# Performance work log

Hardware: AMD Instinct MI355X
Metric: run time of the kernel (lower is better)

## Reference

```python
import jax, jax.numpy as jnp
import numpy as np

EMB = 1024
B, N = 4, 2048


def setup_inputs() -> dict:
    key = jax.random.key(0)
    ks = jax.random.split(key, 10)
    s = 1.0 / np.sqrt(EMB)
    return {
        "x": jax.random.normal(ks[0], (B, N, EMB), dtype=jnp.float32),
        "Wq": jax.random.normal(ks[1], (EMB, EMB), dtype=jnp.float32) * s,
        "bq": jnp.zeros((EMB,), dtype=jnp.float32),
        "Wk": jax.random.normal(ks[2], (EMB, EMB), dtype=jnp.float32) * s,
        "bk": jnp.zeros((EMB,), dtype=jnp.float32),
        "Wv": jax.random.normal(ks[3], (EMB, EMB), dtype=jnp.float32) * s,
        "bv": jnp.zeros((EMB,), dtype=jnp.float32),
        "Wm": jax.random.normal(ks[4], (EMB, EMB), dtype=jnp.float32) * s,
        "bm": jnp.zeros((EMB,), dtype=jnp.float32),
    }


def reference(x, Wq, bq, Wk, bk, Wv, bv, Wm, bm):
    # Projections (torch Linear: x @ W^T + b; here W is stored pre-transposed)
    q = x @ Wq + bq  # [B,N,D]
    k = x @ Wk + bk
    v = x @ Wv + bv
    # scores[b,i,j] = q[b,i,:] . k[b,j,:]  (no 1/sqrt(d) scaling in original)
    scores = jnp.einsum("bid,bjd->bij", q, k)
    # NOTE: softmax over dim=1 (the query/i axis), as in the original
    alpha = jax.nn.softmax(scores, axis=1)  # [B,N,N]
    # t[b,j,d] = sum_i v[b,i,d] * alpha[b,i,j]  == alpha^T @ v per batch
    t = jnp.einsum("bij,bid->bjd", alpha, v)  # [B,N,D]
    # MLP(emb, emb, []) is a single Linear, followed by outer relu
    return jax.nn.relu(t @ Wm + bm)
```

## Files before the change

kernel.cpp:

```cpp
#include <hip/hip_runtime.h>
#include <hip/hip_bf16.h>
#include <hip/hip_fp16.h>
#include <math.h>

#define EMB 1024
#define SEQ 2048
#define BATCH 4

typedef _Float16 half8 __attribute__((ext_vector_type(8)));
typedef float floatx4 __attribute__((ext_vector_type(4)));

__device__ __forceinline__ void gload_lds16(const void* g, void* l) {
    __builtin_amdgcn_global_load_lds(
        (const __attribute__((address_space(1))) void*)g,
        (__attribute__((address_space(3))) void*)l, 16, 0, 0);
}

__device__ __forceinline__ void sbar() {
    __builtin_amdgcn_sched_barrier(0);
    __builtin_amdgcn_s_barrier();
    __builtin_amdgcn_sched_barrier(0);
}

template <int EPI>
__global__ __launch_bounds__(512) void gemm_8p(
    const _Float16* __restrict__ A, const _Float16* __restrict__ B,
    void* __restrict__ Cv, const float* __restrict__ bias,
    int M, int N, int K, long sAb, long sBb, long sCb) {
    __shared__ _Float16 lds[3 * 24576];
    const int tid = threadIdx.x;
    const int lane = tid & 63;
    const int wave = tid >> 6;
    const long zb = blockIdx.z;
    A += zb * sAb;
    B += zb * sBb;
    const int bm = blockIdx.x * 256;
    const int bn = blockIdx.y * 128;
    floatx4 acc[4][4];
#pragma unroll
    for (int mi = 0; mi < 4; ++mi)
#pragma unroll
        for (int ni = 0; ni < 4; ++ni) acc[mi][ni] = (floatx4){0.f, 0.f, 0.f, 0.f};

    const int srow = tid >> 3;
    const int ssl = (tid & 7) ^ (srow & 7);
    const _Float16* Ag = A + (long)(bm + srow) * K + ssl * 8;
    const _Float16* Bg = B + (long)(bn + srow) * K + ssl * 8;
    const long K64 = (long)K * 64;
    const int ldst = wave * 512;

    const int wm = (wave >> 1) * 64;
    const int wn = (wave & 1) * 64;
    const int l15 = lane & 15;
    const int x7 = lane & 7;
    const int g4 = lane >> 4;
    const int sl0 = (g4 ^ x7) * 8;
    const int sl1 = ((4 + g4) ^ x7) * 8;
    const int fA0 = (wm + l15) * 64 + sl0;
    const int fA1 = (wm + l15) * 64 + sl1;
    const int fB0 = 16384 + (wn + l15) * 64 + sl0;
    const int fB1 = 16384 + (wn + l15) * 64 + sl1;

#define STG_H0(kt_, so_)                                                       \
    gload_lds16(Ag + (kt_), &lds[(so_) + ldst]);                               \
    gload_lds16(Ag + K64 + (kt_), &lds[(so_) + 4096 + ldst]);                  \
    gload_lds16(Bg + (kt_), &lds[(so_) + 16384 + ldst]);
#define STG_H1(kt_, so_)                                                       \
    gload_lds16(Ag + 2 * K64 + (kt_), &lds[(so_) + 8192 + ldst]);              \
    gload_lds16(Ag + 3 * K64 + (kt_), &lds[(so_) + 12288 + ldst]);             \
    gload_lds16(Bg + K64 + (kt_), &lds[(so_) + 16384 + 4096 + ldst]);

#define PHASE(fa_, fb_, co_, STG_)                                             \
    {                                                                          \
        half8 af[4], bf[4];                                                    \
        _Pragma("unroll") for (int mi = 0; mi < 4; ++mi)                       \
            af[mi] = *(const half8*)&lds[(co_) + (fa_) + mi * 1024];           \
        _Pragma("unroll") for (int ni = 0; ni < 4; ++ni)                       \
            bf[ni] = *(const half8*)&lds[(co_) + (fb_) + ni * 1024];           \
        STG_                                                                   \
        sbar();                                                                \
        asm volatile("s_waitcnt lgkmcnt(0)" ::: "memory");                     \
        __builtin_amdgcn_sched_barrier(0);                                     \
        __builtin_amdgcn_s_setprio(1);                                         \
        _Pragma("unroll") for (int mi = 0; mi < 4; ++mi)                       \
            _Pragma("unroll") for (int ni = 0; ni < 4; ++ni)                   \
                acc[mi][ni] = __builtin_amdgcn_mfma_f32_16x16x32_f16(          \
                    af[mi], bf[ni], acc[mi][ni], 0, 0, 0);                     \
        __builtin_amdgcn_s_setprio(0);                                         \
    }

#define TILE_END(n_)                                                           \
    __builtin_amdgcn_sched_barrier(0);                                         \
    asm volatile("s_waitcnt vmcnt(" #n_ ")" ::: "memory");                     \
    __builtin_amdgcn_s_barrier();                                              \
    __builtin_amdgcn_sched_barrier(0);

    STG_H0(0, 0) STG_H1(0, 0)
    STG_H0(64, 24576) STG_H1(64, 24576)
    TILE_END(6)
    int co = 0, so = 49152;
    const int NT = K >> 6;
    for (int t = 0; t < NT - 2; ++t) {
        const long kt2 = (long)(t + 2) << 6;
        PHASE(fA0, fB0, co, STG_H0(kt2, so))
        sbar();
        PHASE(fA1, fB1, co, STG_H1(kt2, so))
        TILE_END(6)
        co += 24576; if (co == 73728) co = 0;
        so += 24576; if (so == 73728) so = 0;
    }
    PHASE(fA0, fB0, co, )
    sbar();
    PHASE(fA1, fB1, co, )
    TILE_END(0)
    co += 24576; if (co == 73728) co = 0;
    PHASE(fA0, fB0, co, )
    sbar();
    PHASE(fA1, fB1, co, )
#undef STG_H0
#undef STG_H1
#undef PHASE
#undef TILE_END

    const int er = (lane >> 4) * 4;
    const int ec = lane & 15;
#pragma unroll
    for (int mi = 0; mi < 4; ++mi) {
#pragma unroll
        for (int ni = 0; ni < 4; ++ni) {
            const int col = bn + wn + ni * 16 + ec;
#pragma unroll
            for (int r = 0; r < 4; ++r) {
                const int row = bm + wm + mi * 16 + er + r;
                float v = acc[mi][ni][r];
                if (EPI == 0 || EPI == 1 || EPI == 3) v += bias[col];
                if (EPI == 3) v = fmaxf(v, 0.f);
                if (EPI == 0 || EPI == 4) {
                    ((_Float16*)Cv)[zb * sCb + (long)row * N + col] = (_Float16)v;
                } else if (EPI == 1) {
                    const long b = row >> 11;
                    const long i = row & (SEQ - 1);
                    ((_Float16*)Cv)[(b * EMB + col) * SEQ + i] = (_Float16)v;
                } else {
                    ((float*)Cv)[zb * sCb + (long)row * N + col] = v;
                }
            }
        }
    }
}

__global__ __launch_bounds__(256) void softmax_rows(const float* __restrict__ P,
                                                    _Float16* __restrict__ Aout) {
    const long row = blockIdx.x;
    const float* p = P + row * (long)SEQ;
    const int tid = threadIdx.x;
    float4 x0 = ((const float4*)p)[2 * tid];
    float4 x1 = ((const float4*)p)[2 * tid + 1];
    float v[8] = {x0.x, x0.y, x0.z, x0.w, x1.x, x1.y, x1.z, x1.w};
    float m = v[0];
#pragma unroll
    for (int j = 1; j < 8; ++j) m = fmaxf(m, v[j]);
#pragma unroll
    for (int o = 32; o; o >>= 1) m = fmaxf(m, __shfl_xor(m, o));
    __shared__ float rbuf[4];
    __shared__ float sbuf[4];
    const int lane = tid & 63, wv = tid >> 6;
    if (!lane) rbuf[wv] = m;
    __syncthreads();
    m = fmaxf(fmaxf(rbuf[0], rbuf[1]), fmaxf(rbuf[2], rbuf[3]));
    float s = 0.f;
#pragma unroll
    for (int j = 0; j < 8; ++j) {
        v[j] = expf(v[j] - m);
        s += v[j];
    }
#pragma unroll
    for (int o = 32; o; o >>= 1) s += __shfl_xor(s, o);
    if (!lane) sbuf[wv] = s;
    __syncthreads();
    s = sbuf[0] + sbuf[1] + sbuf[2] + sbuf[3];
    const float inv = 1.f / s;
    half8 h;
#pragma unroll
    for (int j = 0; j < 8; ++j) h[j] = (_Float16)(v[j] * inv);
    *(half8*)(Aout + row * (long)SEQ + tid * 8) = h;
}

__global__ __launch_bounds__(256) void cast_x(const float* __restrict__ X,
                                              _Float16* __restrict__ Xh) {
    const long i = (long)(blockIdx.x * 256 + threadIdx.x) * 8;
    float4 a = ((const float4*)(X + i))[0];
    float4 b = ((const float4*)(X + i))[1];
    half8 h;
    h[0] = (_Float16)a.x; h[1] = (_Float16)a.y; h[2] = (_Float16)a.z; h[3] = (_Float16)a.w;
    h[4] = (_Float16)b.x; h[5] = (_Float16)b.y; h[6] = (_Float16)b.z; h[7] = (_Float16)b.w;
    *(half8*)(Xh + i) = h;
}

__global__ __launch_bounds__(256) void transpose_cast(const float* __restrict__ W,
                                                      _Float16* __restrict__ Wt) {
    __shared__ float tile[32][33];
    const int bx = blockIdx.x * 32;
    const int by = blockIdx.y * 32;
    const int tx = threadIdx.x, ty = threadIdx.y;
#pragma unroll
    for (int r = 0; r < 32; r += 8)
        tile[ty + r][tx] = W[(long)(by + ty + r) * EMB + bx + tx];
    __syncthreads();
#pragma unroll
    for (int r = 0; r < 32; r += 8)
        Wt[(long)(bx + ty + r) * EMB + by + tx] = (_Float16)tile[tx][ty + r];
}

extern "C" void kernel_launch(void* const* d_in, const int* in_sizes, int n_in,
                              void* d_out, int out_size, void* d_ws, size_t ws_size,
                              hipStream_t stream) {
    const float* x  = (const float*)d_in[0];
    const float* Wq = (const float*)d_in[1];
    const float* bq = (const float*)d_in[2];
    const float* Wk = (const float*)d_in[3];
    const float* bk = (const float*)d_in[4];
    const float* Wv = (const float*)d_in[5];
    const float* bv = (const float*)d_in[6];
    const float* Wm = (const float*)d_in[7];
    const float* bm = (const float*)d_in[8];
    float* out = (float*)d_out;

    char* ws = (char*)d_ws;
    const long MB = 1l << 20;
    _Float16* xh  = (_Float16*)(ws + 0 * MB);
    _Float16* wqt = (_Float16*)(ws + 16 * MB);
    _Float16* wkt = (_Float16*)(ws + 18 * MB);
    _Float16* wvt = (_Float16*)(ws + 20 * MB);
    _Float16* wmt = (_Float16*)(ws + 22 * MB);
    _Float16* q   = (_Float16*)(ws + 24 * MB);
    _Float16* k   = (_Float16*)(ws + 40 * MB);
    _Float16* vt  = (_Float16*)(ws + 56 * MB);
    _Float16* t   = (_Float16*)(ws + 72 * MB);
    float*    P   = (float*)(ws + 88 * MB);
    _Float16* al  = (_Float16*)(ws + 152 * MB);

    const long MN = (long)BATCH * SEQ;

    cast_x<<<4096, 256, 0, stream>>>(x, xh);
    transpose_cast<<<dim3(32, 32), dim3(32, 8), 0, stream>>>(Wq, wqt);
    transpose_cast<<<dim3(32, 32), dim3(32, 8), 0, stream>>>(Wk, wkt);
    transpose_cast<<<dim3(32, 32), dim3(32, 8), 0, stream>>>(Wv, wvt);
    transpose_cast<<<dim3(32, 32), dim3(32, 8), 0, stream>>>(Wm, wmt);

    gemm_8p<0><<<dim3(32, 8), 512, 0, stream>>>(xh, wqt, q, bq, (int)MN, EMB, EMB, 0, 0, 0);
    gemm_8p<0><<<dim3(32, 8), 512, 0, stream>>>(xh, wkt, k, bk, (int)MN, EMB, EMB, 0, 0, 0);
    gemm_8p<1><<<dim3(32, 8), 512, 0, stream>>>(xh, wvt, vt, bv, (int)MN, EMB, EMB, 0, 0, 0);

    gemm_8p<2><<<dim3(8, 16, BATCH), 512, 0, stream>>>(
        k, q, P, nullptr, SEQ, SEQ, EMB,
        (long)SEQ * EMB, (long)SEQ * EMB, (long)SEQ * SEQ);

    softmax_rows<<<BATCH * SEQ, 256, 0, stream>>>(P, al);

    gemm_8p<4><<<dim3(8, 8, BATCH), 512, 0, stream>>>(
        al, vt, t, nullptr, SEQ, EMB, SEQ,
        (long)SEQ * SEQ, (long)EMB * SEQ, (long)SEQ * EMB);

    gemm_8p<3><<<dim3(32, 8), 512, 0, stream>>>(t, wmt, out, bm, (int)MN, EMB, EMB, 0, 0, 0);
}
```

Measured before the change: 303.3 us.

## Use 256x256 tile GEMM kernel for attention score and value GEMMs

Adds a new gemm256 kernel with a 256x256 output tile per 512-thread block, a 4-stage LDS ring filled by direct global-to-LDS loads with swizzled columns, and K-tile 32. The two batched attention GEMMs (scores and alpha^T·V) switch to it, so each block gets more data reuse and fewer blocks need to be launched. In exchange each thread holds a larger accumulator and the grid is smaller (256 and 128 blocks), which may leave some CUs idle and raise register pressure.

```diff
diff --git a/kernel.cpp b/kernel.cpp
--- a/kernel.cpp
+++ b/kernel.cpp
@@ -20,6 +20,117 @@
     __builtin_amdgcn_sched_barrier(0);
     __builtin_amdgcn_s_barrier();
     __builtin_amdgcn_sched_barrier(0);
+}
+
+template <int EPI>
+__global__ __launch_bounds__(512, 2) void gemm256(
+    const _Float16* __restrict__ A, const _Float16* __restrict__ B,
+    void* __restrict__ Cv, const float* __restrict__ bias,
+    int M, int N, int K, long sAb, long sBb, long sCb) {
+    __shared__ _Float16 lds[65536];
+    const int tid = threadIdx.x;
+    const int lane = tid & 63;
+    const int wave = tid >> 6;
+    const long zb = blockIdx.z;
+    A += zb * sAb;
+    B += zb * sBb;
+    const int bm = blockIdx.x * 256;
+    const int bn = blockIdx.y * 256;
+    floatx4 acc[8][4];
+#pragma unroll
+    for (int j = 0; j < 8; ++j)
+#pragma unroll
+        for (int n = 0; n < 4; ++n) acc[j][n] = (floatx4){0.f, 0.f, 0.f, 0.f};
+
+    const int r2 = tid >> 2;
+    const int scol = ((tid & 3) ^ ((tid >> 3) & 3)) * 8;
+    const _Float16* Ag0 = A + (long)(bm + r2) * K + scol;
+    const _Float16* Ag1 = A + (long)(bm + 128 + r2) * K + scol;
+    const _Float16* Bg0 = B + (long)(bn + r2) * K + scol;
+    const _Float16* Bg1 = B + (long)(bn + 128 + r2) * K + scol;
+
+    const int wm = (wave >> 2) * 128;
+    const int wn = (wave & 3) * 64;
+    const int fr = lane & 15;
+    const int sp = (lane >> 4) ^ ((fr >> 1) & 3);
+    const int fA = (wm + fr) * 32 + sp * 8;
+    const int fB = 8192 + (wn + fr) * 32 + sp * 8;
+
+#define STAGE_T(u_)                                                           \
+    {                                                                         \
+        const int sb_ = ((u_) & 3) * 16384;                                   \
+        const long kt_ = (long)(u_) << 5;                                     \
+        gload_lds16(Ag0 + kt_, &lds[sb_ + wave * 512]);                       \
+        gload_lds16(Ag1 + kt_, &lds[sb_ + 4096 + wave * 512]);                \
+        gload_lds16(Bg0 + kt_, &lds[sb_ + 8192 + wave * 512]);                \
+        gload_lds16(Bg1 + kt_, &lds[sb_ + 12288 + wave * 512]);               \
+    }
+
+#define COMPUTE_T(t_, STG_)                                                   \
+    {                                                                         \
+        const int cb_ = ((t_) & 3) * 16384;                                   \
+        half8 af[8], bf[4];                                                   \
+        _Pragma("unroll") for (int j = 0; j < 8; ++j)                         \
+            af[j] = *(const half8*)&lds[cb_ + fA + j * 512];                  \
+        _Pragma("unroll") for (int n = 0; n < 4; ++n)                         \
+            bf[n] = *(const half8*)&lds[cb_ + fB + n * 512];                  \
+        STG_                                                                  \
+        asm volatile("s_waitcnt lgkmcnt(0)" ::: "memory");                    \
+        __builtin_amdgcn_sched_barrier(0);                                    \
+        __builtin_amdgcn_s_setprio(1);                                        \
+        _Pragma("unroll") for (int j = 0; j < 8; ++j)                         \
+            _Pragma("unroll") for (int n = 0; n < 4; ++n)                     \
+                acc[j][n] = __builtin_amdgcn_mfma_f32_16x16x32_f16(           \
+                    af[j], bf[n], acc[j][n], 0, 0, 0);                        \
+        __builtin_amdgcn_s_setprio(0);                                        \
+    }
+
+#define TILE_END(n_)                                                          \
+    __builtin_amdgcn_sched_barrier(0);                                        \
+    asm volatile("s_waitcnt vmcnt(" #n_ ")" ::: "memory");                    \
+    __builtin_amdgcn_s_barrier();                                             \
+    __builtin_amdgcn_sched_barrier(0);
+
+    const int NT = K >> 5;
+    STAGE_T(0)
+    STAGE_T(1)
+    STAGE_T(2)
+    TILE_END(8)
+    int t = 0;
+    for (; t + 3 < NT; ++t) {
+        COMPUTE_T(t, STAGE_T(t + 3))
+        TILE_END(8)
+    }
+    COMPUTE_T(t, )
+    TILE_END(4)
+    ++t;
+    COMPUTE_T(t, )
+    TILE_END(0)
+    ++t;
+    COMPUTE_T(t, )
+#undef STAGE_T
+#undef COMPUTE_T
+#undef TILE_END
+
+    const int er = (lane >> 4) * 4;
+    const int ec = lane & 15;
+#pragma unroll
+    for (int j = 0; j < 8; ++j) {
+#pragma unroll
+        for (int n = 0; n < 4; ++n) {
+            const int col = bn + wn + n * 16 + ec;
+#pragma unroll
+            for (int r = 0; r < 4; ++r) {
+                const int row = bm + wm + j * 16 + er + r;
+                float v = acc[j][n][r];
+                if (EPI == 4) {
+                    ((_Float16*)Cv)[zb * sCb + (long)row * N + col] = (_Float16)v;
+                } else {
+                    ((float*)Cv)[zb * sCb + (long)row * N + col] = v;
+                }
+            }
+        }
+    }
 }
 
 template <int EPI>
@@ -135,7 +246,7 @@
                 float v = acc[mi][ni][r];
                 if (EPI == 0 || EPI == 1 || EPI == 3) v += bias[col];
                 if (EPI == 3) v = fmaxf(v, 0.f);
-                if (EPI == 0 || EPI == 4) {
+                if (EPI == 0) {
                     ((_Float16*)Cv)[zb * sCb + (long)row * N + col] = (_Float16)v;
                 } else if (EPI == 1) {
                     const long b = row >> 11;
@@ -252,13 +363,13 @@
     gemm_8p<0><<<dim3(32, 8), 512, 0, stream>>>(xh, wkt, k, bk, (int)MN, EMB, EMB, 0, 0, 0);
     gemm_8p<1><<<dim3(32, 8), 512, 0, stream>>>(xh, wvt, vt, bv, (int)MN, EMB, EMB, 0, 0, 0);
 
-    gemm_8p<2><<<dim3(8, 16, BATCH), 512, 0, stream>>>(
+    gemm256<2><<<dim3(8, 8, BATCH), 512, 0, stream>>>(
         k, q, P, nullptr, SEQ, SEQ, EMB,
         (long)SEQ * EMB, (long)SEQ * EMB, (long)SEQ * SEQ);
 
     softmax_rows<<<BATCH * SEQ, 256, 0, stream>>>(P, al);
 
-    gemm_8p<4><<<dim3(8, 8, BATCH), 512, 0, stream>>>(
+    gemm256<4><<<dim3(8, 4, BATCH), 512, 0, stream>>>(
         al, vt, t, nullptr, SEQ, EMB, SEQ,
         (long)SEQ * SEQ, (long)EMB * SEQ, (long)SEQ * EMB);
 
```

Measured after the change: 313.6 us. 1.03x slower.
